# Kernel optimization log

Hardware: AMD Instinct MI355X
Metric: run time of the kernel (lower is better)

The kernel has to match this reference:

```python
import jax, jax.numpy as jnp
import numpy as np

NUM_HEADS = 16


def setup_inputs() -> dict:
    key = jax.random.key(0)
    ks = jax.random.split(key, 3)
    S, B, E = 2048, 4, 1024
    query = jax.random.normal(ks[0], (S, B, E), dtype=jnp.float32)
    # xavier-uniform-ish scale for projection weights
    w_in = jax.random.normal(ks[1], (3 * E, E), dtype=jnp.float32) * (1.0 / np.sqrt(E))
    b_in = jnp.zeros((3 * E,), dtype=jnp.float32)
    w_out = jax.random.normal(ks[2], (E, E), dtype=jnp.float32) * (1.0 / np.sqrt(E))
    b_out = jnp.zeros((E,), dtype=jnp.float32)
    return {"query": query, "w_in": w_in, "b_in": b_in, "w_out": w_out, "b_out": b_out}


def reference(query, w_in, b_in, w_out, b_out):
    # query: [S, B, E] (seq-first, like nn.MultiheadAttention)
    S, B, E = query.shape
    H = NUM_HEADS
    D = E // H
    scaling = float(D) ** -0.5

    # fused in-projection: [S, B, 3E]
    P = jnp.einsum('sbe,fe->sbf', query, w_in) + b_in
    q, k, v = jnp.split(P, 3, axis=-1)
    q = q * scaling

    # split heads -> [S, B, H, D]
    q = q.reshape(S, B, H, D)
    k = k.reshape(S, B, H, D)
    v = v.reshape(S, B, H, D)

    # scores: [B, H, S(tgt), S(src)] — full O(S^2) matrix, as in the original
    scores = jnp.einsum('sbhd,tbhd->bhst', q, k)
    attn = jax.nn.softmax(scores, axis=-1)  # dropout_p = 0.0

    # context: [S, B, H, D] -> [S, B, E]
    ctx = jnp.einsum('bhst,tbhd->sbhd', attn, v).reshape(S, B, E)

    # out projection
    out = jnp.einsum('sbe,fe->sbf', ctx, w_out) + b_out
    return out
```

## Files before the change

### kernel.cpp

```cpp
#include <hip/hip_runtime.h>
#include <hip/hip_bf16.h>

#define SQ  2048
#define NB  4
#define EE  1024
#define NH  16
#define DH  64
#define BH  64
#define MROWS 8192

using bf16x8 = __attribute__((ext_vector_type(8))) short;
using f32x4  = __attribute__((ext_vector_type(4))) float;

#define MFMA16(a,b,c) __builtin_amdgcn_mfma_f32_16x16x32_bf16((a),(b),(c),0,0,0)

__device__ __forceinline__ short f2bf(float f) {
  union { float f; unsigned u; } v; v.f = f;
  unsigned r = (v.u + 0x7FFFu + ((v.u >> 16) & 1u)) >> 16;
  return (short)r;
}

__device__ __forceinline__ unsigned cvtpk_bf16(float lo, float hi) {
  unsigned r;
  asm("v_cvt_pk_bf16_f32 %0, %1, %2" : "=v"(r) : "v"(lo), "v"(hi));
  return r;
}

__device__ __forceinline__ void gload_lds16(const void* g, void* l) {
  __builtin_amdgcn_global_load_lds((__attribute__((address_space(1))) void*)(g),
                                   (__attribute__((address_space(3))) void*)(l),
                                   16, 0, 0);
}

__global__ __launch_bounds__(256) void cvt_f32_bf16(const float* __restrict__ src,
                                                    short* __restrict__ dst, int n4) {
  int i = blockIdx.x * 256 + threadIdx.x;
  int stride = gridDim.x * 256;
  for (; i < n4; i += stride) {
    float4 v = reinterpret_cast<const float4*>(src)[i];
    short4 o;
    o.x = f2bf(v.x); o.y = f2bf(v.y); o.z = f2bf(v.z); o.w = f2bf(v.w);
    reinterpret_cast<short4*>(dst)[i] = o;
  }
}

template<int MODE>
__global__ __launch_bounds__(256) void gemm_bt(const short* __restrict__ A,
                                               const short* __restrict__ B,
                                               const float* __restrict__ bias,
                                               short* __restrict__ obf,
                                               float* __restrict__ of,
                                               int M, int N, int K) {
  __shared__ short As[128 * 64];
  __shared__ short Bs[128 * 64];
  const int tid  = threadIdx.x;
  const int wave = tid >> 6, lane = tid & 63;
  const int g = lane >> 4, qc = lane & 15;
  const int wr = wave >> 1, wc = wave & 1;
  const int m0 = blockIdx.y << 7, n0 = blockIdx.x << 7;

  f32x4 acc[4][4];
  const f32x4 z4 = {0.f, 0.f, 0.f, 0.f};
#pragma unroll
  for (int m = 0; m < 4; ++m)
#pragma unroll
    for (int n = 0; n < 4; ++n) acc[m][n] = z4;

  const int KT = K >> 6;
  for (int kt = 0; kt < KT; ++kt) {
    const int k0 = kt << 6;
    __syncthreads();
#pragma unroll
    for (int ro = 0; ro < 4; ++ro) {
      int slot = ro * 256 + tid;
      int row  = slot >> 3;
      int cb   = (slot & 7) << 4;
      gload_lds16((const char*)A + ((size_t)(m0 + row) * K + k0) * 2 + cb,
                  (char*)As + ro * 4096 + wave * 1024);
      gload_lds16((const char*)B + ((size_t)(n0 + row) * K + k0) * 2 + cb,
                  (char*)Bs + ro * 4096 + wave * 1024);
    }
    __syncthreads();
#pragma unroll
    for (int kk = 0; kk < 2; ++kk) {
      bf16x8 af[4], bfr[4];
#pragma unroll
      for (int m = 0; m < 4; ++m)
        af[m] = *(const bf16x8*)&As[(wr * 64 + m * 16 + qc) * 64 + kk * 32 + g * 8];
#pragma unroll
      for (int n = 0; n < 4; ++n)
        bfr[n] = *(const bf16x8*)&Bs[(wc * 64 + n * 16 + qc) * 64 + kk * 32 + g * 8];
#pragma unroll
      for (int m = 0; m < 4; ++m)
#pragma unroll
        for (int n = 0; n < 4; ++n)
          acc[m][n] = MFMA16(af[m], bfr[n], acc[m][n]);
    }
  }

#pragma unroll
  for (int m = 0; m < 4; ++m) {
#pragma unroll
    for (int n = 0; n < 4; ++n) {
#pragma unroll
      for (int r = 0; r < 4; ++r) {
        int R = m0 + wr * 64 + m * 16 + 4 * g + r;
        int F = n0 + wc * 64 + n * 16 + qc;
        float val = acc[m][n][r] + bias[F];
        if (MODE == 0) {
          int qkv = F >> 10, e = F & 1023;
          if (qkv == 0) val *= 0.18033688011112042f;
          int h = e >> 6, d = e & 63;
          int s = R >> 2, b = R & 3;
          obf[(size_t)(((qkv << 6) + (b << 4) + h) * SQ + s) * DH + d] = f2bf(val);
        } else {
          of[(size_t)R * N + F] = val;
        }
      }
    }
  }
}

__global__ __launch_bounds__(256) void transpose_v(const short* __restrict__ V,
                                                   short* __restrict__ Vt) {
  __shared__ short T[64 * 72];
  const int bh = blockIdx.y, s0 = blockIdx.x << 6;
  const int tid = threadIdx.x;
  const size_t base = (size_t)bh * SQ * DH;
#pragma unroll
  for (int ro = 0; ro < 2; ++ro) {
    int slot = ro * 256 + tid;
    int row  = slot >> 3;
    int c8   = (slot & 7) << 3;
    bf16x8 v = *(const bf16x8*)(V + base + (size_t)(s0 + row) * DH + c8);
#pragma unroll
    for (int j = 0; j < 8; ++j) T[(c8 + j) * 72 + row] = v[j];
  }
  __syncthreads();
#pragma unroll
  for (int ro = 0; ro < 2; ++ro) {
    int slot = ro * 256 + tid;
    int row  = slot >> 3;
    int c8   = (slot & 7) << 3;
    bf16x8 v = *(const bf16x8*)&T[row * 72 + c8];
    *(bf16x8*)(Vt + base + (size_t)row * SQ + s0 + c8) = v;
  }
}

__global__ __launch_bounds__(256) void attn(const short* __restrict__ Q,
                                            const short* __restrict__ K,
                                            const short* __restrict__ Vt,
                                            short* __restrict__ ctx) {
  __shared__ short Ks[64 * 72];
  __shared__ short Vs[64 * 72];
  __shared__ short Ps[4][32 * 72];
  const int bh = blockIdx.y;
  const int q0 = blockIdx.x << 7;
  const int tid = threadIdx.x;
  const int wave = tid >> 6, lane = tid & 63;
  const int g = lane >> 4, qc = lane & 15;
  const size_t base = (size_t)bh * SQ * DH;

  bf16x8 qf[2][2];
#pragma unroll
  for (int qh = 0; qh < 2; ++qh) {
    const short* qr = Q + base + (size_t)(q0 + wave * 32 + qh * 16 + qc) * DH;
    qf[qh][0] = *(const bf16x8*)(qr + g * 8);
    qf[qh][1] = *(const bf16x8*)(qr + 32 + g * 8);
  }

  const f32x4 z4 = {0.f, 0.f, 0.f, 0.f};
  f32x4 acc[4][2];
#pragma unroll
  for (int dt = 0; dt < 4; ++dt) { acc[dt][0] = z4; acc[dt][1] = z4; }
  float mrun[2] = {-3e38f, -3e38f}, lrun[2] = {0.f, 0.f};

  bf16x8 kreg[2], vreg[2];
#define LOADKV(KT_) do { int kv0_ = (KT_) << 6;                                  \
    _Pragma("unroll")                                                            \
    for (int ro = 0; ro < 2; ++ro) {                                             \
      int slot = ro * 256 + tid; int row = slot >> 3; int c8 = (slot & 7) << 3;  \
      kreg[ro] = *(const bf16x8*)(K + base + (size_t)(kv0_ + row) * DH + c8);    \
      vreg[ro] = *(const bf16x8*)(Vt + base + (size_t)row * SQ + kv0_ + c8);     \
    } } while (0)

  LOADKV(0);

  const int NT = SQ / 64;
  for (int kt = 0; kt < NT; ++kt) {
    __syncthreads();
#pragma unroll
    for (int ro = 0; ro < 2; ++ro) {
      int slot = ro * 256 + tid; int row = slot >> 3; int c8 = (slot & 7) << 3;
      *(bf16x8*)&Ks[row * 72 + c8] = kreg[ro];
      *(bf16x8*)&Vs[row * 72 + c8] = vreg[ro];
    }
    __syncthreads();
    int nx = kt + 1 < NT - 1 ? kt + 1 : NT - 1;
    LOADKV(nx);

    f32x4 sc[2][4];
#pragma unroll
    for (int t = 0; t < 4; ++t) {
      bf16x8 kf0 = *(const bf16x8*)&Ks[(t * 16 + qc) * 72 + g * 8];
      bf16x8 kf1 = *(const bf16x8*)&Ks[(t * 16 + qc) * 72 + 32 + g * 8];
      sc[0][t] = MFMA16(kf1, qf[0][1], MFMA16(kf0, qf[0][0], z4));
      sc[1][t] = MFMA16(kf1, qf[1][1], MFMA16(kf0, qf[1][0], z4));
    }

#pragma unroll
    for (int qh = 0; qh < 2; ++qh) {
      float pmax = -3e38f;
#pragma unroll
      for (int t = 0; t < 4; ++t)
#pragma unroll
        for (int r = 0; r < 4; ++r) pmax = fmaxf(pmax, sc[qh][t][r]);
      pmax = fmaxf(pmax, __shfl_xor(pmax, 16));
      pmax = fmaxf(pmax, __shfl_xor(pmax, 32));

      float mnew = mrun[qh];
      if (!__all(pmax - mrun[qh] <= 11.0f)) {
        mnew = fmaxf(mrun[qh], pmax);
        float alpha = exp2f(mrun[qh] - mnew);
        float a_r[4];
#pragma unroll
        for (int r = 0; r < 4; ++r) a_r[r] = __shfl(alpha, 4 * g + r);
#pragma unroll
        for (int dt = 0; dt < 4; ++dt) {
          acc[dt][qh][0] *= a_r[0]; acc[dt][qh][1] *= a_r[1];
          acc[dt][qh][2] *= a_r[2]; acc[dt][qh][3] *= a_r[3];
        }
        lrun[qh] *= alpha;
        mrun[qh] = mnew;
      }

      float psum = 0.f;
#pragma unroll
      for (int t = 0; t < 4; ++t) {
        float p0 = exp2f(sc[qh][t][0] - mnew);
        float p1 = exp2f(sc[qh][t][1] - mnew);
        float p2 = exp2f(sc[qh][t][2] - mnew);
        float p3 = exp2f(sc[qh][t][3] - mnew);
        psum += (p0 + p1) + (p2 + p3);
        uint2 w;
        w.x = cvtpk_bf16(p0, p1);
        w.y = cvtpk_bf16(p2, p3);
        *(uint2*)&Ps[wave][(qh * 16 + qc) * 72 + t * 16 + g * 4] = w;
      }
      psum += __shfl_xor(psum, 16);
      psum += __shfl_xor(psum, 32);
      lrun[qh] += psum;
    }

    bf16x8 pa[2][2];
#pragma unroll
    for (int qh = 0; qh < 2; ++qh) {
      pa[qh][0] = *(const bf16x8*)&Ps[wave][(qh * 16 + qc) * 72 + g * 8];
      pa[qh][1] = *(const bf16x8*)&Ps[wave][(qh * 16 + qc) * 72 + 32 + g * 8];
    }
#pragma unroll
    for (int dt = 0; dt < 4; ++dt) {
      bf16x8 vf0 = *(const bf16x8*)&Vs[(dt * 16 + qc) * 72 + g * 8];
      bf16x8 vf1 = *(const bf16x8*)&Vs[(dt * 16 + qc) * 72 + 32 + g * 8];
#pragma unroll
      for (int qh = 0; qh < 2; ++qh) {
        acc[dt][qh] = MFMA16(pa[qh][0], vf0, acc[dt][qh]);
        acc[dt][qh] = MFMA16(pa[qh][1], vf1, acc[dt][qh]);
      }
    }
  }
#undef LOADKV

  const int b_ = bh >> 4, h = bh & 15;
#pragma unroll
  for (int qh = 0; qh < 2; ++qh) {
    float linv = 1.f / lrun[qh];
    float l_r[4];
#pragma unroll
    for (int r = 0; r < 4; ++r) l_r[r] = __shfl(linv, 4 * g + r);
#pragma unroll
    for (int dt = 0; dt < 4; ++dt) {
#pragma unroll
      for (int r = 0; r < 4; ++r) {
        int s = q0 + wave * 32 + qh * 16 + 4 * g + r;
        int e = h * 64 + dt * 16 + qc;
        ctx[(size_t)(s * 4 + b_) * EE + e] = f2bf(acc[dt][qh][r] * l_r[r]);
      }
    }
  }
}

extern "C" void kernel_launch(void* const* d_in, const int* in_sizes, int n_in,
                              void* d_out, int out_size, void* d_ws, size_t ws_size,
                              hipStream_t stream) {
  const float* query = (const float*)d_in[0];
  const float* w_in  = (const float*)d_in[1];
  const float* b_in  = (const float*)d_in[2];
  const float* w_out = (const float*)d_in[3];
  const float* b_out = (const float*)d_in[4];
  float* out = (float*)d_out;

  char* ws = (char*)d_ws;
  short* Xbf  = (short*)(ws);
  short* Wbf  = (short*)(ws + (size_t)(16 << 20));
  short* WObf = (short*)(ws + (size_t)(22 << 20));
  short* QKV  = (short*)(ws + (size_t)(24 << 20));
  short* Vt   = (short*)(ws + (size_t)(72 << 20));
  short* ctx  = Xbf;

  cvt_f32_bf16<<<1024, 256, 0, stream>>>(query, Xbf, (SQ * NB * EE) / 4);
  cvt_f32_bf16<<<512, 256, 0, stream>>>(w_in, Wbf, (3 * EE * EE) / 4);
  cvt_f32_bf16<<<256, 256, 0, stream>>>(w_out, WObf, (EE * EE) / 4);

  gemm_bt<0><<<dim3(24, 64), 256, 0, stream>>>(Xbf, Wbf, b_in, QKV, nullptr,
                                               MROWS, 3 * EE, EE);
  transpose_v<<<dim3(32, 64), 256, 0, stream>>>(QKV + 2 * (size_t)8388608, Vt);
  attn<<<dim3(16, 64), 256, 0, stream>>>(QKV, QKV + (size_t)8388608, Vt, ctx);
  gemm_bt<1><<<dim3(8, 64), 256, 0, stream>>>(ctx, WObf, b_out, nullptr, out,
                                              MROWS, EE, EE);
}
```

Before: 354.8 us.

## Rewrite attention inner loop with 32x32 MFMA and register-resident P

The attention kernel now uses 32x32x16 bf16 MFMA with a transposed formulation, so each lane owns one query row. Softmax row max and sum then reduce mostly in registers. P is repacked with permlane32 swaps and fed straight into the PV MFMA, which removes the per-wave LDS round trip for P. K and V tiles are double-buffered in XOR-swizzled LDS, which cuts one barrier per iteration and avoids bank conflicts without padding. Output stores become packed bf16 writes, and launch bounds request 3 blocks per CU. The risk is higher register pressure from the 16-wide accumulators and correctness of the permlane layout.

```diff
diff --git a/kernel.cpp b/kernel.cpp
--- a/kernel.cpp
+++ b/kernel.cpp
@@ -11,8 +11,10 @@
 
 using bf16x8 = __attribute__((ext_vector_type(8))) short;
 using f32x4  = __attribute__((ext_vector_type(4))) float;
+using f32x16 = __attribute__((ext_vector_type(16))) float;
 
 #define MFMA16(a,b,c) __builtin_amdgcn_mfma_f32_16x16x32_bf16((a),(b),(c),0,0,0)
+#define MFMA32(a,b,c) __builtin_amdgcn_mfma_f32_32x32x16_bf16((a),(b),(c),0,0,0)
 
 __device__ __forceinline__ short f2bf(float f) {
   union { float f; unsigned u; } v; v.f = f;
@@ -147,146 +149,147 @@
   }
 }
 
-__global__ __launch_bounds__(256) void attn(const short* __restrict__ Q,
-                                            const short* __restrict__ K,
-                                            const short* __restrict__ Vt,
-                                            short* __restrict__ ctx) {
-  __shared__ short Ks[64 * 72];
-  __shared__ short Vs[64 * 72];
-  __shared__ short Ps[4][32 * 72];
+__global__ __launch_bounds__(256, 3) void attn(const short* __restrict__ Q,
+                                               const short* __restrict__ K,
+                                               const short* __restrict__ Vt,
+                                               short* __restrict__ ctx) {
+  __shared__ short Ks[2][64 * 64];
+  __shared__ short Vs[2][64 * 64];
   const int bh = blockIdx.y;
   const int q0 = blockIdx.x << 7;
   const int tid = threadIdx.x;
-  const int wave = tid >> 6, lane = tid & 63;
-  const int g = lane >> 4, qc = lane & 15;
+  const int wq = tid >> 6, lane = tid & 63;
+  const int col = lane & 31, hi = lane >> 5;
   const size_t base = (size_t)bh * SQ * DH;
-
-  bf16x8 qf[2][2];
-#pragma unroll
-  for (int qh = 0; qh < 2; ++qh) {
-    const short* qr = Q + base + (size_t)(q0 + wave * 32 + qh * 16 + qc) * DH;
-    qf[qh][0] = *(const bf16x8*)(qr + g * 8);
-    qf[qh][1] = *(const bf16x8*)(qr + 32 + g * 8);
-  }
-
-  const f32x4 z4 = {0.f, 0.f, 0.f, 0.f};
-  f32x4 acc[4][2];
-#pragma unroll
-  for (int dt = 0; dt < 4; ++dt) { acc[dt][0] = z4; acc[dt][1] = z4; }
-  float mrun[2] = {-3e38f, -3e38f}, lrun[2] = {0.f, 0.f};
+  const int qrow = q0 + wq * 32 + col;
+
+  bf16x8 qf[4];
+  {
+    const short* qr = Q + base + (size_t)qrow * DH + hi * 8;
+#pragma unroll
+    for (int kd = 0; kd < 4; ++kd) qf[kd] = *(const bf16x8*)(qr + kd * 16);
+  }
+
+  f32x16 acc0 = {0.f,0.f,0.f,0.f,0.f,0.f,0.f,0.f,0.f,0.f,0.f,0.f,0.f,0.f,0.f,0.f};
+  f32x16 acc1 = acc0;
+  float m = -3e38f, l = 0.f;
 
   bf16x8 kreg[2], vreg[2];
 #define LOADKV(KT_) do { int kv0_ = (KT_) << 6;                                  \
     _Pragma("unroll")                                                            \
     for (int ro = 0; ro < 2; ++ro) {                                             \
-      int slot = ro * 256 + tid; int row = slot >> 3; int c8 = (slot & 7) << 3;  \
-      kreg[ro] = *(const bf16x8*)(K + base + (size_t)(kv0_ + row) * DH + c8);    \
-      vreg[ro] = *(const bf16x8*)(Vt + base + (size_t)row * SQ + kv0_ + c8);     \
+      int slot = ro * 256 + tid; int row = slot >> 3; int cs = (slot & 7) << 3;  \
+      kreg[ro] = *(const bf16x8*)(K + base + (size_t)(kv0_ + row) * DH + cs);    \
+      vreg[ro] = *(const bf16x8*)(Vt + base + (size_t)row * SQ + kv0_ + cs);     \
     } } while (0)
 
   LOADKV(0);
 
+  const int swz = (col & 7) << 3;
   const int NT = SQ / 64;
   for (int kt = 0; kt < NT; ++kt) {
+    const int bb = kt & 1;
+#pragma unroll
+    for (int ro = 0; ro < 2; ++ro) {
+      int slot = ro * 256 + tid; int row = slot >> 3; int cs = (slot & 7) << 3;
+      int so = row * 64 + (cs ^ ((row & 7) << 3));
+      *(bf16x8*)&Ks[bb][so] = kreg[ro];
+      *(bf16x8*)&Vs[bb][so] = vreg[ro];
+    }
     __syncthreads();
-#pragma unroll
-    for (int ro = 0; ro < 2; ++ro) {
-      int slot = ro * 256 + tid; int row = slot >> 3; int c8 = (slot & 7) << 3;
-      *(bf16x8*)&Ks[row * 72 + c8] = kreg[ro];
-      *(bf16x8*)&Vs[row * 72 + c8] = vreg[ro];
-    }
-    __syncthreads();
-    int nx = kt + 1 < NT - 1 ? kt + 1 : NT - 1;
+    int nx = kt + 1 < NT ? kt + 1 : kt;
     LOADKV(nx);
 
-    f32x4 sc[2][4];
-#pragma unroll
-    for (int t = 0; t < 4; ++t) {
-      bf16x8 kf0 = *(const bf16x8*)&Ks[(t * 16 + qc) * 72 + g * 8];
-      bf16x8 kf1 = *(const bf16x8*)&Ks[(t * 16 + qc) * 72 + 32 + g * 8];
-      sc[0][t] = MFMA16(kf1, qf[0][1], MFMA16(kf0, qf[0][0], z4));
-      sc[1][t] = MFMA16(kf1, qf[1][1], MFMA16(kf0, qf[1][0], z4));
-    }
-
-#pragma unroll
-    for (int qh = 0; qh < 2; ++qh) {
-      float pmax = -3e38f;
-#pragma unroll
-      for (int t = 0; t < 4; ++t)
-#pragma unroll
-        for (int r = 0; r < 4; ++r) pmax = fmaxf(pmax, sc[qh][t][r]);
-      pmax = fmaxf(pmax, __shfl_xor(pmax, 16));
-      pmax = fmaxf(pmax, __shfl_xor(pmax, 32));
-
-      float mnew = mrun[qh];
-      if (!__all(pmax - mrun[qh] <= 11.0f)) {
-        mnew = fmaxf(mrun[qh], pmax);
-        float alpha = exp2f(mrun[qh] - mnew);
-        float a_r[4];
-#pragma unroll
-        for (int r = 0; r < 4; ++r) a_r[r] = __shfl(alpha, 4 * g + r);
-#pragma unroll
-        for (int dt = 0; dt < 4; ++dt) {
-          acc[dt][qh][0] *= a_r[0]; acc[dt][qh][1] *= a_r[1];
-          acc[dt][qh][2] *= a_r[2]; acc[dt][qh][3] *= a_r[3];
-        }
-        lrun[qh] *= alpha;
-        mrun[qh] = mnew;
+    f32x16 s0 = {0.f,0.f,0.f,0.f,0.f,0.f,0.f,0.f,0.f,0.f,0.f,0.f,0.f,0.f,0.f,0.f};
+    f32x16 s1 = s0;
+#pragma unroll
+    for (int kd = 0; kd < 4; ++kd) {
+      bf16x8 k0 = *(const bf16x8*)&Ks[bb][col * 64 + ((kd * 16 + hi * 8) ^ swz)];
+      s0 = MFMA32(k0, qf[kd], s0);
+    }
+#pragma unroll
+    for (int kd = 0; kd < 4; ++kd) {
+      bf16x8 k1 = *(const bf16x8*)&Ks[bb][(32 + col) * 64 + ((kd * 16 + hi * 8) ^ swz)];
+      s1 = MFMA32(k1, qf[kd], s1);
+    }
+
+    float t16[16];
+#pragma unroll
+    for (int i = 0; i < 16; ++i) t16[i] = fmaxf(s0[i], s1[i]);
+#pragma unroll
+    for (int i = 0; i < 8; ++i) t16[i] = fmaxf(t16[i], t16[i + 8]);
+#pragma unroll
+    for (int i = 0; i < 4; ++i) t16[i] = fmaxf(t16[i], t16[i + 4]);
+    float pmax = fmaxf(fmaxf(t16[0], t16[1]), fmaxf(t16[2], t16[3]));
+    pmax = fmaxf(pmax, __shfl_xor(pmax, 32));
+
+    float mnew = m;
+    if (!__all(pmax - m <= 11.0f)) {
+      mnew = fmaxf(m, pmax);
+      float alpha = exp2f(m - mnew);
+#pragma unroll
+      for (int i = 0; i < 16; ++i) { acc0[i] *= alpha; acc1[i] *= alpha; }
+      l *= alpha;
+      m = mnew;
+    }
+
+    float p[32];
+#pragma unroll
+    for (int i = 0; i < 16; ++i) p[i] = exp2f(s0[i] - mnew);
+#pragma unroll
+    for (int i = 0; i < 16; ++i) p[16 + i] = exp2f(s1[i] - mnew);
+    float a16[16];
+#pragma unroll
+    for (int i = 0; i < 16; ++i) a16[i] = p[i] + p[16 + i];
+#pragma unroll
+    for (int i = 0; i < 8; ++i) a16[i] += a16[i + 8];
+#pragma unroll
+    for (int i = 0; i < 4; ++i) a16[i] += a16[i + 4];
+    float psum = (a16[0] + a16[1]) + (a16[2] + a16[3]);
+    psum += __shfl_xor(psum, 32);
+    l += psum;
+
+    union PW { unsigned u[4]; bf16x8 v; };
+    PW pw[4];
+#pragma unroll
+    for (int h2 = 0; h2 < 2; ++h2) {
+#pragma unroll
+      for (int c = 0; c < 2; ++c) {
+        int bx = h2 * 16 + c * 8;
+        unsigned x0 = cvtpk_bf16(p[bx + 0], p[bx + 1]);
+        unsigned x1 = cvtpk_bf16(p[bx + 2], p[bx + 3]);
+        unsigned y0 = cvtpk_bf16(p[bx + 4], p[bx + 5]);
+        unsigned y1 = cvtpk_bf16(p[bx + 6], p[bx + 7]);
+        asm("v_permlane32_swap_b32 %0, %1" : "+v"(x0), "+v"(y0));
+        asm("v_permlane32_swap_b32 %0, %1" : "+v"(x1), "+v"(y1));
+        pw[h2 * 2 + c].u[0] = x0; pw[h2 * 2 + c].u[1] = x1;
+        pw[h2 * 2 + c].u[2] = y0; pw[h2 * 2 + c].u[3] = y1;
       }
-
-      float psum = 0.f;
-#pragma unroll
-      for (int t = 0; t < 4; ++t) {
-        float p0 = exp2f(sc[qh][t][0] - mnew);
-        float p1 = exp2f(sc[qh][t][1] - mnew);
-        float p2 = exp2f(sc[qh][t][2] - mnew);
-        float p3 = exp2f(sc[qh][t][3] - mnew);
-        psum += (p0 + p1) + (p2 + p3);
-        uint2 w;
-        w.x = cvtpk_bf16(p0, p1);
-        w.y = cvtpk_bf16(p2, p3);
-        *(uint2*)&Ps[wave][(qh * 16 + qc) * 72 + t * 16 + g * 4] = w;
-      }
-      psum += __shfl_xor(psum, 16);
-      psum += __shfl_xor(psum, 32);
-      lrun[qh] += psum;
-    }
-
-    bf16x8 pa[2][2];
-#pragma unroll
-    for (int qh = 0; qh < 2; ++qh) {
-      pa[qh][0] = *(const bf16x8*)&Ps[wave][(qh * 16 + qc) * 72 + g * 8];
-      pa[qh][1] = *(const bf16x8*)&Ps[wave][(qh * 16 + qc) * 72 + 32 + g * 8];
-    }
-#pragma unroll
-    for (int dt = 0; dt < 4; ++dt) {
-      bf16x8 vf0 = *(const bf16x8*)&Vs[(dt * 16 + qc) * 72 + g * 8];
-      bf16x8 vf1 = *(const bf16x8*)&Vs[(dt * 16 + qc) * 72 + 32 + g * 8];
-#pragma unroll
-      for (int qh = 0; qh < 2; ++qh) {
-        acc[dt][qh] = MFMA16(pa[qh][0], vf0, acc[dt][qh]);
-        acc[dt][qh] = MFMA16(pa[qh][1], vf1, acc[dt][qh]);
-      }
+    }
+
+#pragma unroll
+    for (int cc = 0; cc < 4; ++cc) {
+      bf16x8 vf0 = *(const bf16x8*)&Vs[bb][col * 64 + ((cc * 16 + hi * 8) ^ swz)];
+      acc0 = MFMA32(vf0, pw[cc].v, acc0);
+      bf16x8 vf1 = *(const bf16x8*)&Vs[bb][(32 + col) * 64 + ((cc * 16 + hi * 8) ^ swz)];
+      acc1 = MFMA32(vf1, pw[cc].v, acc1);
     }
   }
 #undef LOADKV
 
+  float li = 1.f / l;
   const int b_ = bh >> 4, h = bh & 15;
-#pragma unroll
-  for (int qh = 0; qh < 2; ++qh) {
-    float linv = 1.f / lrun[qh];
-    float l_r[4];
-#pragma unroll
-    for (int r = 0; r < 4; ++r) l_r[r] = __shfl(linv, 4 * g + r);
-#pragma unroll
-    for (int dt = 0; dt < 4; ++dt) {
-#pragma unroll
-      for (int r = 0; r < 4; ++r) {
-        int s = q0 + wave * 32 + qh * 16 + 4 * g + r;
-        int e = h * 64 + dt * 16 + qc;
-        ctx[(size_t)(s * 4 + b_) * EE + e] = f2bf(acc[dt][qh][r] * l_r[r]);
-      }
-    }
+  short* orow = ctx + (size_t)(qrow * 4 + b_) * EE + h * 64;
+#pragma unroll
+  for (int t = 0; t < 4; ++t) {
+    int d0 = 8 * t + 4 * hi;
+    uint2 w0, w1;
+    w0.x = cvtpk_bf16(acc0[4 * t + 0] * li, acc0[4 * t + 1] * li);
+    w0.y = cvtpk_bf16(acc0[4 * t + 2] * li, acc0[4 * t + 3] * li);
+    *(uint2*)(orow + d0) = w0;
+    w1.x = cvtpk_bf16(acc1[4 * t + 0] * li, acc1[4 * t + 1] * li);
+    w1.y = cvtpk_bf16(acc1[4 * t + 2] * li, acc1[4 * t + 3] * li);
+    *(uint2*)(orow + 32 + d0) = w1;
   }
 }
 
```

Result: faster. 345.1 us (-2.7%).
